# Optimization experiments

Hardware: AMD Instinct MI355X
Metric: run time of the kernel (lower is better)

The kernel has to match this reference:

```python
import math
import jax, jax.numpy as jnp
import numpy as np

EPS = 1e-5
D_MODEL, N_HEADS, D_HEAD = 512, 8, 64


def make_signed_quant(num_bits):
    Qn = -2 ** (num_bits - 1)
    Qp = 2 ** (num_bits - 1) - 1

    @jax.custom_vjp
    def quant(x, alpha):
        a = jnp.maximum(alpha, EPS)
        return jnp.clip(jnp.round(x / a), Qn, Qp) * a

    def fwd(x, alpha):
        a = jnp.maximum(alpha, EPS)
        return jnp.clip(jnp.round(x / a), Qn, Qp) * a, (x, a)

    def bwd(res, g):
        x, a = res
        qw = x / a
        small = (qw < Qn).astype(g.dtype)
        big = (qw > Qp).astype(g.dtype)
        mid = 1.0 - small - big
        gs = 1.0 / math.sqrt(x.size * Qp)
        ga = jnp.sum((small * Qn + big * Qp + mid * (jnp.round(qw) - qw)) * g) * gs
        return mid * g, ga.reshape(())

    quant.defvjp(fwd, bwd)
    return quant


def make_unsigned_quant(num_bits):
    Qp = 2 ** num_bits - 1

    @jax.custom_vjp
    def quant(x, alpha):
        a = jnp.maximum(alpha, EPS)
        mn = jnp.min(x)
        return jnp.clip(jnp.round((x - mn) / a), 0, Qp) * a + mn

    def fwd(x, alpha):
        a = jnp.maximum(alpha, EPS)
        mn = jnp.min(x)
        return jnp.clip(jnp.round((x - mn) / a), 0, Qp) * a + mn, (x - mn, a)

    def bwd(res, g):
        xs, a = res
        qw = xs / a
        small = (qw < 0).astype(g.dtype)
        big = (qw > Qp).astype(g.dtype)
        mid = 1.0 - small - big
        gs = 1.0 / math.sqrt(xs.size * Qp)
        ga = jnp.sum((big * Qp + mid * (jnp.round(qw) - qw)) * g) * gs
        return mid * g, ga.reshape(())

    quant.defvjp(fwd, bwd)
    return quant


def _bwn_body(w):
    # layerwise BWN: sign(w - mean(w)) * mean(|w|)
    m = jnp.mean(jnp.abs(w))
    e = jnp.mean(w)
    return jnp.sign(w - e) * m


@jax.custom_vjp
def bwn(w):
    return _bwn_body(w)


def _bwn_fwd(w):
    return _bwn_body(w), None


def _bwn_bwd(_, g):
    return (g,)  # straight-through


bwn.defvjp(_bwn_fwd, _bwn_bwd)

sig4 = make_signed_quant(4)
sig8 = make_signed_quant(8)  # the output QuantizeLinear uses default input_bits=8
uns4 = make_unsigned_quant(4)


def layernorm(x, g, b):
    mu = jnp.mean(x, axis=-1, keepdims=True)
    var = jnp.var(x, axis=-1, keepdims=True)
    return (x - mu) / jnp.sqrt(var + 1e-5) * g + b


def attention_forward(q, k, v, Wq, Wk, Wv, Wo, bq, bk, bv, ln_g, ln_b,
                      aq_in, ak_in, av_in, a_cq, a_ck, a_cv, a_cattn, ao_in):
    B, S, _ = q.shape
    # QuantizeLinear: 4-bit elastic act quant + BWN binary weights, NO bias; then LearnableBias add
    Q = sig4(q, aq_in) @ bwn(Wq).T + bq
    K = sig4(k, ak_in) @ bwn(Wk).T + bk
    V = sig4(v, av_in) @ bwn(Wv).T + bv

    def split(x):  # [B,S,H*d] -> [B,H,S,d]
        return jnp.transpose(x.reshape(B, -1, N_HEADS, D_HEAD), (0, 2, 1, 3))

    Q, K, V = split(Q), split(K), split(V)
    Q = sig4(Q, a_cq)
    K = sig4(K, a_ck)
    V = sig4(V, a_cv)
    scores = jnp.einsum('bhqd,bhkd->bhqk', Q, K) / math.sqrt(D_HEAD)
    # NOTE: original calls scores.masked_fill(mask==0, -1e9) WITHOUT assignment,
    # so the mask has no effect on the math; replicated faithfully.
    attn = jax.nn.softmax(scores, axis=-1)
    attn = uns4(attn, a_cattn)
    ctx = jnp.einsum('bhqk,bhkd->bhqd', attn, V)
    # faithful to original `.view(B, S, H*d)` on the [B,H,S,d] tensor (no head transpose)
    ctx = ctx.reshape(B, S, N_HEADS * D_HEAD)
    out = sig8(ctx, ao_in) @ bwn(Wo).T
    return layernorm(q + out, ln_g, ln_b), scores


def setup_inputs() -> dict:
    key = jax.random.key(0)
    ks = jax.random.split(key, 8)
    B, S, D = 4, 1024, 512
    f = jnp.float32
    return {
        'q': jax.random.normal(ks[0], (B, S, D), f),
        'k': jax.random.normal(ks[1], (B, S, D), f),
        'v': jax.random.normal(ks[2], (B, S, D), f),
        'mask': jnp.ones((B, 1, S, S), jnp.int32),
        'Wq': jax.random.normal(ks[3], (D, D), f) * 0.02,
        'Wk': jax.random.normal(ks[4], (D, D), f) * 0.02,
        'Wv': jax.random.normal(ks[5], (D, D), f) * 0.02,
        'Wo': jax.random.normal(ks[6], (D, D), f) * 0.02,
        'bq': jnp.zeros((D,), f),
        'bk': jnp.zeros((D,), f),
        'bv': jnp.zeros((D,), f),
        'ln_g': jnp.ones((D,), f),
        'ln_b': jnp.zeros((D,), f),
        'aq_in': jnp.asarray(0.5, f),
        'ak_in': jnp.asarray(0.5, f),
        'av_in': jnp.asarray(0.5, f),
        'a_cq': jnp.asarray(0.2, f),
        'a_ck': jnp.asarray(0.2, f),
        'a_cv': jnp.asarray(0.2, f),
        'a_cattn': jnp.asarray(0.002, f),
        'ao_in': jnp.asarray(0.01, f),
    }


def reference(q, k, v, mask, Wq, Wk, Wv, Wo, bq, bk, bv, ln_g, ln_b,
              aq_in, ak_in, av_in, a_cq, a_ck, a_cv, a_cattn, ao_in):
    # mask is structurally unused (original masked_fill is not in-place and discarded)
    return attention_forward(q, k, v, Wq, Wk, Wv, Wo, bq, bk, bv, ln_g, ln_b,
                             aq_in, ak_in, av_in, a_cq, a_ck, a_cv, a_cattn, ao_in)
```

## Files before the change

### kernel.cpp

```cpp
#include <hip/hip_runtime.h>
#include <math.h>
#include <stdint.h>

#define EPSQ 1e-5f
#define WELEM 262144
#define OUT0N 2097152

#define O_WSUM   0
#define O_WABS   16
#define O_MN     32
#define O_COLSUM 64
#define O_WSIGNS 16384
#define O_QLV    (O_WSIGNS + 8*WELEM)
#define O_CTXQ   O_QLV
#define O_KLV    (O_QLV + 4194304)
#define O_VLV    (O_KLV + 4194304)
#define O_KQ     (O_VLV + 4194304)
#define O_KK     (O_KQ + 4194304)
#define O_VT     (O_KK + 4194304)
#define O_RMAX   (O_VT + 4194304)
#define O_RSUM   (O_RMAX + 131072)
#define O_OUTB   (O_RSUM + 131072)
#define O_RCAND  O_OUTB

#define AS 72

typedef __bf16 bf16x8 __attribute__((ext_vector_type(8)));
typedef __bf16 bf16x4 __attribute__((ext_vector_type(4)));
typedef float  floatx4 __attribute__((ext_vector_type(4)));

struct pre2 { bf16x8 lo, hi; };
__device__ __forceinline__ pre2 ldb16(const __bf16* p) {
  pre2 r; r.lo = *(const bf16x8*)p; r.hi = *(const bf16x8*)(p + 8); return r;
}
__device__ __forceinline__ void stb16(__bf16* p, pre2 r) {
  *(bf16x8*)p = r.lo; *(bf16x8*)(p + 8) = r.hi;
}

__device__ __forceinline__ float clampf(float x, float lo, float hi) {
  return fminf(fmaxf(x, lo), hi);
}

__global__ void k_init(float* wsum, float* wabs, float* colsum) {
  int t = threadIdx.x;
  if (t < 4) { wsum[t] = 0.f; wabs[t] = 0.f; }
  for (int i = t; i < 2048; i += 256) colsum[i] = 0.f;
}

__global__ void k_wstats(const float* Wq, const float* Wk, const float* Wv, const float* Wo,
                         float* wsum, float* wabs) {
  __shared__ float s1[256], s2[256];
  int w = blockIdx.x >> 6;
  const float* W = (w == 0) ? Wq : (w == 1) ? Wk : (w == 2) ? Wv : Wo;
  int base = (blockIdx.x & 63) * 4096;
  float s = 0.f, sa = 0.f;
  for (int i = threadIdx.x; i < 4096; i += 256) {
    float x = W[base + i];
    s += x; sa += fabsf(x);
  }
  s1[threadIdx.x] = s; s2[threadIdx.x] = sa; __syncthreads();
  for (int o = 128; o > 0; o >>= 1) {
    if (threadIdx.x < o) { s1[threadIdx.x] += s1[threadIdx.x + o]; s2[threadIdx.x] += s2[threadIdx.x + o]; }
    __syncthreads();
  }
  if (threadIdx.x == 0) { atomicAdd(&wsum[w], s1[0]); atomicAdd(&wabs[w], s2[0]); }
}

__global__ void k_sign(const float* Wq, const float* Wk, const float* Wv, const float* Wo,
                       const float* wsum, __bf16* wsigns) {
  int idx = blockIdx.x * 256 + threadIdx.x;
  int w = idx >> 18;
  int pos = idx & (WELEM - 1);
  const float* W = (w == 0) ? Wq : (w == 1) ? Wk : (w == 2) ? Wv : Wo;
  float e = wsum[w] * (1.0f / 262144.0f);
  float x = W[pos];
  wsigns[idx] = (__bf16)(float)((x > e) - (x < e));
}

__global__ __launch_bounds__(256) void k_qx(
    const float* q, const float* kin, const float* vin,
    const float* aq, const float* ak, const float* av,
    __bf16* qlv, __bf16* klv, __bf16* vlv) {
  int z = blockIdx.y;
  const float* X = (z == 0) ? q : (z == 1) ? kin : vin;
  const float* ap = (z == 0) ? aq : (z == 1) ? ak : av;
  __bf16* O = (z == 0) ? qlv : (z == 1) ? klv : vlv;
  float a = fmaxf(ap[0], EPSQ);
  size_t i = ((size_t)blockIdx.x * 256 + threadIdx.x) * 8;
  float4 x0 = *(const float4*)&X[i];
  float4 x1 = *(const float4*)&X[i + 4];
  bf16x8 o = { (__bf16)clampf(rintf(x0.x / a), -8.f, 7.f),
               (__bf16)clampf(rintf(x0.y / a), -8.f, 7.f),
               (__bf16)clampf(rintf(x0.z / a), -8.f, 7.f),
               (__bf16)clampf(rintf(x0.w / a), -8.f, 7.f),
               (__bf16)clampf(rintf(x1.x / a), -8.f, 7.f),
               (__bf16)clampf(rintf(x1.y / a), -8.f, 7.f),
               (__bf16)clampf(rintf(x1.z / a), -8.f, 7.f),
               (__bf16)clampf(rintf(x1.w / a), -8.f, 7.f) };
  *(bf16x8*)&O[i] = o;
}

__global__ __launch_bounds__(256) void k_proj(
    const __bf16* qlv, const __bf16* klv, const __bf16* vlv,
    const float* bq, const float* bk, const float* bv,
    const float* aq, const float* ak, const float* av,
    const float* acq, const float* ack, const float* acv,
    const __bf16* wsigns, const float* wabs,
    __bf16* kqo, __bf16* kko, __bf16* vto, float* colsum) {
  __shared__ __align__(16) __bf16 As[64][AS];
  __shared__ __align__(16) __bf16 Bs[64][AS];
  int z = blockIdx.z;
  const __bf16* X   = (z == 0) ? qlv : (z == 1) ? klv : vlv;
  const float* bias = (z == 0) ? bq  : (z == 1) ? bk  : bv;
  const float* aip  = (z == 0) ? aq  : (z == 1) ? ak  : av;
  const float* ahp  = (z == 0) ? acq : (z == 1) ? ack : acv;
  float a_in = fmaxf(aip[0], EPSQ);
  float a_hd = fmaxf(ahp[0], EPSQ);
  float m_w  = wabs[z] * (1.0f / 262144.0f);
  const __bf16* S = wsigns + (size_t)z * WELEM;

  int n0 = blockIdx.x * 64;
  int f0 = blockIdx.y * 64;
  int t = threadIdx.x;
  int lane = t & 63, w = t >> 6, quad = lane >> 4, l16 = lane & 15;
  int e16 = (t & 3) * 16, mrow = t >> 2;
  const __bf16* ap = &X[(size_t)(n0 + mrow) * 512 + e16];
  const __bf16* bp = &S[(size_t)(f0 + mrow) * 512 + e16];
  floatx4 acc[4];
#pragma unroll
  for (int nt = 0; nt < 4; ++nt) acc[nt] = (floatx4){0.f, 0.f, 0.f, 0.f};

  pre2 pa = ldb16(ap), pb = ldb16(bp);
  for (int k0 = 0; k0 < 512; k0 += 64) {
    if (k0) __syncthreads();
    stb16(&As[mrow][e16], pa);
    stb16(&Bs[mrow][e16], pb);
    if (k0 + 64 < 512) { pa = ldb16(ap + k0 + 64); pb = ldb16(bp + k0 + 64); }
    __syncthreads();
#pragma unroll
    for (int kh = 0; kh < 64; kh += 32) {
      bf16x8 a = *(const bf16x8*)&As[w * 16 + l16][kh + quad * 8];
#pragma unroll
      for (int nt = 0; nt < 4; ++nt) {
        bf16x8 b = *(const bf16x8*)&Bs[nt * 16 + l16][kh + quad * 8];
        acc[nt] = __builtin_amdgcn_mfma_f32_16x16x32_bf16(a, b, acc[nt], 0, 0, 0);
      }
    }
  }
  float s_am = a_in * m_w;
  if (z != 2) {
    __bf16* outp = (z == 0) ? kqo : kko;
#pragma unroll
    for (int nt = 0; nt < 4; ++nt) {
      int f = f0 + nt * 16 + l16;
      int h = f >> 6, dd = f & 63;
      float bia = bias[f];
#pragma unroll
      for (int r = 0; r < 4; ++r) {
        int n = n0 + w * 16 + quad * 4 + r;
        int b = n >> 10, srow = n & 1023;
        float P = s_am * acc[nt][r] + bia;
        float hq = clampf(rintf(P / a_hd), -8.f, 7.f);
        outp[(size_t)((b * 8 + h) * 1024 + srow) * 64 + dd] = (__bf16)hq;
      }
    }
  } else {
    int b = n0 >> 10;
    int srow0 = (n0 & 1023) + w * 16 + quad * 4;
#pragma unroll
    for (int nt = 0; nt < 4; ++nt) {
      int f = f0 + nt * 16 + l16;
      int h = f >> 6, dd = f & 63;
      int bh = b * 8 + h;
      float bia = bias[f];
      float part = 0.f;
      bf16x4 pack;
#pragma unroll
      for (int r = 0; r < 4; ++r) {
        float P = s_am * acc[nt][r] + bia;
        float hq = clampf(rintf(P / a_hd), -8.f, 7.f);
        pack[r] = (__bf16)hq;
        part += hq;
      }
      *(bf16x4*)&vto[((size_t)bh * 64 + dd) * 1024 + srow0] = pack;
      atomicAdd(&colsum[bh * 64 + dd], part);
    }
  }
}

__global__ __launch_bounds__(256) void k_qks(
    const __bf16* kq, const __bf16* kkv,
    const float* acq, const float* ack,
    float* scores, float* rmax, float* rsum, float* rcand) {
  __shared__ __align__(16) __bf16 As[64][AS];
  __shared__ __align__(16) __bf16 Bs[64][AS];
  int bh = blockIdx.y;
  int q0 = blockIdx.x * 64;
  const __bf16* A  = kq  + (size_t)bh * 65536;
  const __bf16* Bp = kkv + (size_t)bh * 65536;
  float* Sp = scores + ((size_t)bh * 1024 + q0) * 1024;
  int t = threadIdx.x;
  int lane = t & 63, w = t >> 6, quad = lane >> 4, l16 = lane & 15;
  int e16 = (t & 3) * 16, mrow = t >> 2;
  float sc = fmaxf(acq[0], EPSQ) * fmaxf(ack[0], EPSQ) * 0.125f;

  stb16(&As[mrow][e16], ldb16(&A[(q0 + mrow) * 64 + e16]));
  float m_run[4], l_run[4], mn_run[4];
#pragma unroll
  for (int rr = 0; rr < 4; ++rr) { m_run[rr] = -INFINITY; l_run[rr] = 0.f; mn_run[rr] = INFINITY; }

  pre2 pb = ldb16(&Bp[mrow * 64 + e16]);
  for (int ct = 0; ct < 16; ++ct) {
    if (ct) __syncthreads();
    stb16(&Bs[mrow][e16], pb);
    if (ct < 15) pb = ldb16(&Bp[((ct + 1) * 64 + mrow) * 64 + e16]);
    __syncthreads();
    floatx4 acc[4];
#pragma unroll
    for (int nt = 0; nt < 4; ++nt) acc[nt] = (floatx4){0.f, 0.f, 0.f, 0.f};
#pragma unroll
    for (int kh = 0; kh < 64; kh += 32) {
      bf16x8 a = *(const bf16x8*)&As[w * 16 + l16][kh + quad * 8];
#pragma unroll
      for (int nt = 0; nt < 4; ++nt) {
        bf16x8 b = *(const bf16x8*)&Bs[nt * 16 + l16][kh + quad * 8];
        acc[nt] = __builtin_amdgcn_mfma_f32_16x16x32_bf16(a, b, acc[nt], 0, 0, 0);
      }
    }
#pragma unroll
    for (int rr = 0; rr < 4; ++rr) {
      int row = w * 16 + quad * 4 + rr;
      float v[4];
#pragma unroll
      for (int nt = 0; nt < 4; ++nt) {
        v[nt] = sc * acc[nt][rr];
        Sp[(size_t)row * 1024 + ct * 64 + nt * 16 + l16] = v[nt];
      }
      float tmax = fmaxf(fmaxf(v[0], v[1]), fmaxf(v[2], v[3]));
      float tmin = fminf(fminf(v[0], v[1]), fminf(v[2], v[3]));
      mn_run[rr] = fminf(mn_run[rr], tmin);
      float mnew = fmaxf(m_run[rr], tmax);
      float s = 0.f;
#pragma unroll
      for (int nt = 0; nt < 4; ++nt) s += expf(v[nt] - mnew);
      l_run[rr] = l_run[rr] * expf(m_run[rr] - mnew) + s;
      m_run[rr] = mnew;
    }
  }
#pragma unroll
  for (int o = 1; o < 16; o <<= 1) {
#pragma unroll
    for (int rr = 0; rr < 4; ++rr) {
      float mo = __shfl_xor(m_run[rr], o);
      float lo = __shfl_xor(l_run[rr], o);
      float mnew = fmaxf(m_run[rr], mo);
      l_run[rr] = l_run[rr] * expf(m_run[rr] - mnew) + lo * expf(mo - mnew);
      m_run[rr] = mnew;
      mn_run[rr] = fminf(mn_run[rr], __shfl_xor(mn_run[rr], o));
    }
  }
  if (l16 == 0) {
#pragma unroll
    for (int rr = 0; rr < 4; ++rr) {
      int r = bh * 1024 + q0 + w * 16 + quad * 4 + rr;
      rmax[r] = m_run[rr];
      rsum[r] = l_run[rr];
      rcand[r] = expf(mn_run[rr] - m_run[rr]) * (1.0f / l_run[rr]);
    }
  }
}

__global__ __launch_bounds__(1024) void k_minred(const float* rcand, float* mnf) {
  __shared__ float red[1024];
  float mn = INFINITY;
  for (int i = threadIdx.x; i < 32768; i += 1024) mn = fminf(mn, rcand[i]);
  red[threadIdx.x] = mn; __syncthreads();
  for (int o = 512; o > 0; o >>= 1) {
    if (threadIdx.x < o) red[threadIdx.x] = fminf(red[threadIdx.x], red[threadIdx.x + o]);
    __syncthreads();
  }
  if (threadIdx.x == 0) mnf[0] = red[0];
}

__global__ __launch_bounds__(256) void k_pv(
    const float* scores, const float* rmax, const float* rsum,
    const float* mnf, const float* colsum, const __bf16* vt,
    const float* acattn, const float* acv, const float* ao,
    __bf16* ctxq) {
  __shared__ __align__(16) __bf16 As[32][AS];
  __shared__ __align__(16) __bf16 Bs[64][AS];
  int bh = blockIdx.y;
  int m0 = blockIdx.x * 32;
  float mn = mnf[0];
  float a_att = fmaxf(acattn[0], EPSQ);
  float a_v   = fmaxf(acv[0], EPSQ);
  float a_o   = fmaxf(ao[0], EPSQ);
  const float* Sp  = scores + (size_t)bh * 1048576;
  const __bf16* Vt = vt + (size_t)bh * 65536;
  int t = threadIdx.x;
  int lane = t & 63, w = t >> 6, quad = lane >> 4, l16 = lane & 15;
  int mt = w & 1, np = w >> 1;
  int c4 = (t & 15) * 4, mb = t >> 4;
  int e16 = (t & 3) * 16, mrow = t >> 2;
  float rm[2], rs[2];
#pragma unroll
  for (int j = 0; j < 2; ++j) {
    int r = bh * 1024 + m0 + mb + j * 16;
    rm[j] = rmax[r]; rs[j] = rsum[r];
  }
  floatx4 acc[2];
  acc[0] = (floatx4){0.f, 0.f, 0.f, 0.f};
  acc[1] = (floatx4){0.f, 0.f, 0.f, 0.f};

  float4 ps[2];
#pragma unroll
  for (int j = 0; j < 2; ++j)
    ps[j] = *(const float4*)&Sp[(size_t)(m0 + mb + j * 16) * 1024 + c4];
  pre2 pvb = ldb16(&Vt[(size_t)mrow * 1024 + e16]);

  for (int k0 = 0; k0 < 1024; k0 += 64) {
    if (k0) __syncthreads();
#pragma unroll
    for (int j = 0; j < 2; ++j) {
      float inv = 1.0f / rs[j];
      bf16x4 av = {
        (__bf16)clampf(rintf((expf(ps[j].x - rm[j]) * inv - mn) / a_att), 0.f, 15.f),
        (__bf16)clampf(rintf((expf(ps[j].y - rm[j]) * inv - mn) / a_att), 0.f, 15.f),
        (__bf16)clampf(rintf((expf(ps[j].z - rm[j]) * inv - mn) / a_att), 0.f, 15.f),
        (__bf16)clampf(rintf((expf(ps[j].w - rm[j]) * inv - mn) / a_att), 0.f, 15.f) };
      *(bf16x4*)&As[mb + j * 16][c4] = av;
    }
    stb16(&Bs[mrow][e16], pvb);
    if (k0 + 64 < 1024) {
#pragma unroll
      for (int j = 0; j < 2; ++j)
        ps[j] = *(const float4*)&Sp[(size_t)(m0 + mb + j * 16) * 1024 + k0 + 64 + c4];
      pvb = ldb16(&Vt[(size_t)mrow * 1024 + k0 + 64 + e16]);
    }
    __syncthreads();
#pragma unroll
    for (int kh = 0; kh < 64; kh += 32) {
      bf16x8 a = *(const bf16x8*)&As[mt * 16 + l16][kh + quad * 8];
#pragma unroll
      for (int j = 0; j < 2; ++j) {
        bf16x8 b = *(const bf16x8*)&Bs[(np * 2 + j) * 16 + l16][kh + quad * 8];
        acc[j] = __builtin_amdgcn_mfma_f32_16x16x32_bf16(a, b, acc[j], 0, 0, 0);
      }
    }
  }
  float sc  = a_att * a_v;
  float mnv = mn * a_v;
  int b = bh >> 3, h = bh & 7;
#pragma unroll
  for (int j = 0; j < 2; ++j) {
    int dd = (np * 2 + j) * 16 + l16;
    float cs = colsum[bh * 64 + dd];
#pragma unroll
    for (int r = 0; r < 4; ++r) {
      int srow = m0 + mt * 16 + quad * 4 + r;
      float ctx = sc * acc[j][r] + mnv * cs;
      float c8 = clampf(rintf(ctx / a_o), -128.f, 127.f);
      ctxq[(size_t)b * 524288 + (size_t)(h * 128 + (srow >> 3)) * 512 + (srow & 7) * 64 + dd] = (__bf16)c8;
    }
  }
}

__global__ __launch_bounds__(256) void k_outg(
    const __bf16* ctxq, const __bf16* signs_o,
    const float* wabs, const float* ao, float* outb) {
  __shared__ __align__(16) __bf16 As[64][AS];
  __shared__ __align__(16) __bf16 Bs[64][AS];
  int n0 = blockIdx.x * 64, f0 = blockIdx.y * 64;
  int t = threadIdx.x;
  int lane = t & 63, w = t >> 6, quad = lane >> 4, l16 = lane & 15;
  int e16 = (t & 3) * 16, mrow = t >> 2;
  const __bf16* ap = &ctxq[(size_t)(n0 + mrow) * 512 + e16];
  const __bf16* bp = &signs_o[(size_t)(f0 + mrow) * 512 + e16];
  floatx4 acc[4];
#pragma unroll
  for (int nt = 0; nt < 4; ++nt) acc[nt] = (floatx4){0.f, 0.f, 0.f, 0.f};
  pre2 pa = ldb16(ap), pb = ldb16(bp);
  for (int k0 = 0; k0 < 512; k0 += 64) {
    if (k0) __syncthreads();
    stb16(&As[mrow][e16], pa);
    stb16(&Bs[mrow][e16], pb);
    if (k0 + 64 < 512) { pa = ldb16(ap + k0 + 64); pb = ldb16(bp + k0 + 64); }
    __syncthreads();
#pragma unroll
    for (int kh = 0; kh < 64; kh += 32) {
      bf16x8 a = *(const bf16x8*)&As[w * 16 + l16][kh + quad * 8];
#pragma unroll
      for (int nt = 0; nt < 4; ++nt) {
        bf16x8 b = *(const bf16x8*)&Bs[nt * 16 + l16][kh + quad * 8];
        acc[nt] = __builtin_amdgcn_mfma_f32_16x16x32_bf16(a, b, acc[nt], 0, 0, 0);
      }
    }
  }
  float scale = fmaxf(ao[0], EPSQ) * (wabs[3] * (1.0f / 262144.0f));
#pragma unroll
  for (int nt = 0; nt < 4; ++nt)
#pragma unroll
    for (int r = 0; r < 4; ++r)
      outb[(size_t)(n0 + w * 16 + quad * 4 + r) * 512 + f0 + nt * 16 + l16] = scale * acc[nt][r];
}

__global__ __launch_bounds__(256) void k_ln(
    const float* q, const float* outb, const float* g, const float* bb, float* out0) {
  __shared__ float red[256];
  int r = blockIdx.x, t = threadIdx.x;
  const float* qp = q + (size_t)r * 512;
  const float* op = outb + (size_t)r * 512;
  float y0 = qp[t] + op[t];
  float y1 = qp[t + 256] + op[t + 256];
  red[t] = y0 + y1; __syncthreads();
  for (int o = 128; o > 0; o >>= 1) { if (t < o) red[t] += red[t + o]; __syncthreads(); }
  float mu = red[0] * (1.0f / 512.0f); __syncthreads();
  float d0 = y0 - mu, d1 = y1 - mu;
  red[t] = d0 * d0 + d1 * d1; __syncthreads();
  for (int o = 128; o > 0; o >>= 1) { if (t < o) red[t] += red[t + o]; __syncthreads(); }
  float var = red[0] * (1.0f / 512.0f);
  float den = sqrtf(var + 1e-5f);
  out0[(size_t)r * 512 + t]       = d0 / den * g[t] + bb[t];
  out0[(size_t)r * 512 + t + 256] = d1 / den * g[t + 256] + bb[t + 256];
}

extern "C" void kernel_launch(void* const* d_in, const int* in_sizes, int n_in,
                              void* d_out, int out_size, void* d_ws, size_t ws_size,
                              hipStream_t stream) {
  const float* q   = (const float*)d_in[0];
  const float* k   = (const float*)d_in[1];
  const float* v   = (const float*)d_in[2];
  const float* Wq  = (const float*)d_in[4];
  const float* Wk  = (const float*)d_in[5];
  const float* Wv  = (const float*)d_in[6];
  const float* Wo  = (const float*)d_in[7];
  const float* bq  = (const float*)d_in[8];
  const float* bk  = (const float*)d_in[9];
  const float* bv  = (const float*)d_in[10];
  const float* lng = (const float*)d_in[11];
  const float* lnb = (const float*)d_in[12];
  const float* aq  = (const float*)d_in[13];
  const float* ak  = (const float*)d_in[14];
  const float* av  = (const float*)d_in[15];
  const float* acq = (const float*)d_in[16];
  const float* ack = (const float*)d_in[17];
  const float* acv = (const float*)d_in[18];
  const float* aca = (const float*)d_in[19];
  const float* ao  = (const float*)d_in[20];

  char* ws = (char*)d_ws;
  float*  wsum   = (float*)(ws + O_WSUM);
  float*  wabs   = (float*)(ws + O_WABS);
  float*  mnf    = (float*)(ws + O_MN);
  float*  colsum = (float*)(ws + O_COLSUM);
  __bf16* wsigns = (__bf16*)(ws + O_WSIGNS);
  __bf16* qlv    = (__bf16*)(ws + O_QLV);
  __bf16* klv    = (__bf16*)(ws + O_KLV);
  __bf16* vlv    = (__bf16*)(ws + O_VLV);
  __bf16* kqb    = (__bf16*)(ws + O_KQ);
  __bf16* kkb    = (__bf16*)(ws + O_KK);
  __bf16* vtb    = (__bf16*)(ws + O_VT);
  float*  rmax   = (float*)(ws + O_RMAX);
  float*  rsum   = (float*)(ws + O_RSUM);
  float*  rcand  = (float*)(ws + O_RCAND);
  __bf16* ctxq   = (__bf16*)(ws + O_CTXQ);
  float*  outb   = (float*)(ws + O_OUTB);

  float* out0   = (float*)d_out;
  float* scores = (float*)d_out + OUT0N;

  k_init<<<1, 256, 0, stream>>>(wsum, wabs, colsum);
  k_wstats<<<256, 256, 0, stream>>>(Wq, Wk, Wv, Wo, wsum, wabs);
  k_sign<<<4096, 256, 0, stream>>>(Wq, Wk, Wv, Wo, wsum, wsigns);
  k_qx<<<dim3(1024, 3), 256, 0, stream>>>(q, k, v, aq, ak, av, qlv, klv, vlv);
  k_proj<<<dim3(64, 8, 3), 256, 0, stream>>>(qlv, klv, vlv, bq, bk, bv, aq, ak, av,
                                             acq, ack, acv, wsigns, wabs,
                                             kqb, kkb, vtb, colsum);
  k_qks<<<dim3(16, 32), 256, 0, stream>>>(kqb, kkb, acq, ack, scores, rmax, rsum, rcand);
  k_minred<<<1, 1024, 0, stream>>>(rcand, mnf);
  k_pv<<<dim3(32, 32), 256, 0, stream>>>(scores, rmax, rsum, mnf, colsum, vtb,
                                         aca, acv, ao, ctxq);
  k_outg<<<dim3(64, 8), 256, 0, stream>>>(ctxq, wsigns + 3 * WELEM, wabs, ao, outb);
  k_ln<<<4096, 256, 0, stream>>>(q, outb, lng, lnb, out0);
}
```

Before: 349.3 us.

## Recompute QK scores in PV kernel and fuse global min via atomicMin

```diff
diff --git a/kernel.cpp b/kernel.cpp
--- a/kernel.cpp
+++ b/kernel.cpp
@@ -21,7 +21,6 @@
 #define O_RMAX   (O_VT + 4194304)
 #define O_RSUM   (O_RMAX + 131072)
 #define O_OUTB   (O_RSUM + 131072)
-#define O_RCAND  O_OUTB
 
 #define AS 72
 
@@ -41,9 +40,10 @@
   return fminf(fmaxf(x, lo), hi);
 }
 
-__global__ void k_init(float* wsum, float* wabs, float* colsum) {
+__global__ void k_init(float* wsum, float* wabs, float* colsum, unsigned int* mnbits) {
   int t = threadIdx.x;
   if (t < 4) { wsum[t] = 0.f; wabs[t] = 0.f; }
+  if (t == 0) mnbits[0] = 0x7f800000u;
   for (int i = t; i < 2048; i += 256) colsum[i] = 0.f;
 }
 
@@ -191,9 +191,10 @@
 __global__ __launch_bounds__(256) void k_qks(
     const __bf16* kq, const __bf16* kkv,
     const float* acq, const float* ack,
-    float* scores, float* rmax, float* rsum, float* rcand) {
+    float* scores, float* rmax, float* rsum, unsigned int* mnbits) {
   __shared__ __align__(16) __bf16 As[64][AS];
   __shared__ __align__(16) __bf16 Bs[64][AS];
+  __shared__ float redmin[16];
   int bh = blockIdx.y;
   int q0 = blockIdx.x * 64;
   const __bf16* A  = kq  + (size_t)bh * 65536;
@@ -260,95 +261,112 @@
     }
   }
   if (l16 == 0) {
+    float cand = INFINITY;
 #pragma unroll
     for (int rr = 0; rr < 4; ++rr) {
       int r = bh * 1024 + q0 + w * 16 + quad * 4 + rr;
       rmax[r] = m_run[rr];
       rsum[r] = l_run[rr];
-      rcand[r] = expf(mn_run[rr] - m_run[rr]) * (1.0f / l_run[rr]);
-    }
-  }
-}
-
-__global__ __launch_bounds__(1024) void k_minred(const float* rcand, float* mnf) {
-  __shared__ float red[1024];
-  float mn = INFINITY;
-  for (int i = threadIdx.x; i < 32768; i += 1024) mn = fminf(mn, rcand[i]);
-  red[threadIdx.x] = mn; __syncthreads();
-  for (int o = 512; o > 0; o >>= 1) {
-    if (threadIdx.x < o) red[threadIdx.x] = fminf(red[threadIdx.x], red[threadIdx.x + o]);
-    __syncthreads();
-  }
-  if (threadIdx.x == 0) mnf[0] = red[0];
+      cand = fminf(cand, expf(mn_run[rr] - m_run[rr]) * (1.0f / l_run[rr]));
+    }
+    redmin[w * 4 + quad] = cand;
+  }
+  __syncthreads();
+  if (t == 0) {
+    float c = redmin[0];
+#pragma unroll
+    for (int i = 1; i < 16; ++i) c = fminf(c, redmin[i]);
+    atomicMin(mnbits, __float_as_uint(c));
+  }
 }
 
 __global__ __launch_bounds__(256) void k_pv(
-    const float* scores, const float* rmax, const float* rsum,
+    const __bf16* kq, const __bf16* kkv,
+    const float* rmax, const float* rsum,
     const float* mnf, const float* colsum, const __bf16* vt,
+    const float* acq, const float* ack,
     const float* acattn, const float* acv, const float* ao,
     __bf16* ctxq) {
+  __shared__ __align__(16) __bf16 Ks[64][AS];
+  __shared__ __align__(16) __bf16 Vs[64][AS];
   __shared__ __align__(16) __bf16 As[32][AS];
-  __shared__ __align__(16) __bf16 Bs[64][AS];
   int bh = blockIdx.y;
   int m0 = blockIdx.x * 32;
-  float mn = mnf[0];
+  float mn    = mnf[0];
   float a_att = fmaxf(acattn[0], EPSQ);
   float a_v   = fmaxf(acv[0], EPSQ);
   float a_o   = fmaxf(ao[0], EPSQ);
-  const float* Sp  = scores + (size_t)bh * 1048576;
-  const __bf16* Vt = vt + (size_t)bh * 65536;
+  float sc    = fmaxf(acq[0], EPSQ) * fmaxf(ack[0], EPSQ) * 0.125f;
+  const __bf16* Qp = kq  + (size_t)bh * 65536;
+  const __bf16* Kp = kkv + (size_t)bh * 65536;
+  const __bf16* Vt = vt  + (size_t)bh * 65536;
   int t = threadIdx.x;
   int lane = t & 63, w = t >> 6, quad = lane >> 4, l16 = lane & 15;
+  int e16 = (t & 3) * 16, mrow = t >> 2;
   int mt = w & 1, np = w >> 1;
-  int c4 = (t & 15) * 4, mb = t >> 4;
-  int e16 = (t & 3) * 16, mrow = t >> 2;
-  float rm[2], rs[2];
-#pragma unroll
-  for (int j = 0; j < 2; ++j) {
-    int r = bh * 1024 + m0 + mb + j * 16;
-    rm[j] = rmax[r]; rs[j] = rsum[r];
-  }
+
+  bf16x8 qa[2][2];
+#pragma unroll
+  for (int mh = 0; mh < 2; ++mh)
+#pragma unroll
+    for (int kh2 = 0; kh2 < 2; ++kh2)
+      qa[mh][kh2] = *(const bf16x8*)&Qp[(size_t)(m0 + mh * 16 + l16) * 64 + kh2 * 32 + quad * 8];
+
+  float rm[2][4], inv[2][4];
+#pragma unroll
+  for (int mh = 0; mh < 2; ++mh)
+#pragma unroll
+    for (int r = 0; r < 4; ++r) {
+      int rr = bh * 1024 + m0 + mh * 16 + quad * 4 + r;
+      rm[mh][r]  = rmax[rr];
+      inv[mh][r] = 1.0f / rsum[rr];
+    }
+
   floatx4 acc[2];
   acc[0] = (floatx4){0.f, 0.f, 0.f, 0.f};
   acc[1] = (floatx4){0.f, 0.f, 0.f, 0.f};
 
-  float4 ps[2];
-#pragma unroll
-  for (int j = 0; j < 2; ++j)
-    ps[j] = *(const float4*)&Sp[(size_t)(m0 + mb + j * 16) * 1024 + c4];
-  pre2 pvb = ldb16(&Vt[(size_t)mrow * 1024 + e16]);
-
-  for (int k0 = 0; k0 < 1024; k0 += 64) {
-    if (k0) __syncthreads();
-#pragma unroll
-    for (int j = 0; j < 2; ++j) {
-      float inv = 1.0f / rs[j];
-      bf16x4 av = {
-        (__bf16)clampf(rintf((expf(ps[j].x - rm[j]) * inv - mn) / a_att), 0.f, 15.f),
-        (__bf16)clampf(rintf((expf(ps[j].y - rm[j]) * inv - mn) / a_att), 0.f, 15.f),
-        (__bf16)clampf(rintf((expf(ps[j].z - rm[j]) * inv - mn) / a_att), 0.f, 15.f),
-        (__bf16)clampf(rintf((expf(ps[j].w - rm[j]) * inv - mn) / a_att), 0.f, 15.f) };
-      *(bf16x4*)&As[mb + j * 16][c4] = av;
-    }
-    stb16(&Bs[mrow][e16], pvb);
-    if (k0 + 64 < 1024) {
-#pragma unroll
-      for (int j = 0; j < 2; ++j)
-        ps[j] = *(const float4*)&Sp[(size_t)(m0 + mb + j * 16) * 1024 + k0 + 64 + c4];
-      pvb = ldb16(&Vt[(size_t)mrow * 1024 + k0 + 64 + e16]);
-    }
+  pre2 kpre = ldb16(&Kp[(size_t)mrow * 64 + e16]);
+  pre2 vpre = ldb16(&Vt[(size_t)mrow * 1024 + e16]);
+  for (int ct = 0; ct < 16; ++ct) {
+    if (ct) __syncthreads();
+    stb16(&Ks[mrow][e16], kpre);
+    stb16(&Vs[mrow][e16], vpre);
+    if (ct < 15) {
+      kpre = ldb16(&Kp[(size_t)((ct + 1) * 64 + mrow) * 64 + e16]);
+      vpre = ldb16(&Vt[(size_t)mrow * 1024 + (ct + 1) * 64 + e16]);
+    }
+    __syncthreads();
+    floatx4 s2[2];
+    s2[0] = (floatx4){0.f, 0.f, 0.f, 0.f};
+    s2[1] = (floatx4){0.f, 0.f, 0.f, 0.f};
+#pragma unroll
+    for (int kh2 = 0; kh2 < 2; ++kh2) {
+      bf16x8 b = *(const bf16x8*)&Ks[w * 16 + l16][kh2 * 32 + quad * 8];
+#pragma unroll
+      for (int mh = 0; mh < 2; ++mh)
+        s2[mh] = __builtin_amdgcn_mfma_f32_16x16x32_bf16(qa[mh][kh2], b, s2[mh], 0, 0, 0);
+    }
+#pragma unroll
+    for (int mh = 0; mh < 2; ++mh)
+#pragma unroll
+      for (int r = 0; r < 4; ++r) {
+        float p = expf(sc * s2[mh][r] - rm[mh][r]) * inv[mh][r];
+        As[mh * 16 + quad * 4 + r][w * 16 + l16] =
+            (__bf16)clampf(rintf((p - mn) / a_att), 0.f, 15.f);
+      }
     __syncthreads();
 #pragma unroll
     for (int kh = 0; kh < 64; kh += 32) {
       bf16x8 a = *(const bf16x8*)&As[mt * 16 + l16][kh + quad * 8];
 #pragma unroll
       for (int j = 0; j < 2; ++j) {
-        bf16x8 b = *(const bf16x8*)&Bs[(np * 2 + j) * 16 + l16][kh + quad * 8];
+        bf16x8 b = *(const bf16x8*)&Vs[(np * 2 + j) * 16 + l16][kh + quad * 8];
         acc[j] = __builtin_amdgcn_mfma_f32_16x16x32_bf16(a, b, acc[j], 0, 0, 0);
       }
     }
   }
-  float sc  = a_att * a_v;
+  float scf = a_att * a_v;
   float mnv = mn * a_v;
   int b = bh >> 3, h = bh & 7;
 #pragma unroll
@@ -358,7 +376,7 @@
 #pragma unroll
     for (int r = 0; r < 4; ++r) {
       int srow = m0 + mt * 16 + quad * 4 + r;
-      float ctx = sc * acc[j][r] + mnv * cs;
+      float ctx = scf * acc[j][r] + mnv * cs;
       float c8 = clampf(rintf(ctx / a_o), -128.f, 127.f);
       ctxq[(size_t)b * 524288 + (size_t)(h * 128 + (srow >> 3)) * 512 + (srow & 7) * 64 + dd] = (__bf16)c8;
     }
@@ -462,24 +480,23 @@
   __bf16* vtb    = (__bf16*)(ws + O_VT);
   float*  rmax   = (float*)(ws + O_RMAX);
   float*  rsum   = (float*)(ws + O_RSUM);
-  float*  rcand  = (float*)(ws + O_RCAND);
   __bf16* ctxq   = (__bf16*)(ws + O_CTXQ);
   float*  outb   = (float*)(ws + O_OUTB);
 
   float* out0   = (float*)d_out;
   float* scores = (float*)d_out + OUT0N;
 
-  k_init<<<1, 256, 0, stream>>>(wsum, wabs, colsum);
+  k_init<<<1, 256, 0, stream>>>(wsum, wabs, colsum, (unsigned int*)mnf);
   k_wstats<<<256, 256, 0, stream>>>(Wq, Wk, Wv, Wo, wsum, wabs);
   k_sign<<<4096, 256, 0, stream>>>(Wq, Wk, Wv, Wo, wsum, wsigns);
   k_qx<<<dim3(1024, 3), 256, 0, stream>>>(q, k, v, aq, ak, av, qlv, klv, vlv);
   k_proj<<<dim3(64, 8, 3), 256, 0, stream>>>(qlv, klv, vlv, bq, bk, bv, aq, ak, av,
                                              acq, ack, acv, wsigns, wabs,
                                              kqb, kkb, vtb, colsum);
-  k_qks<<<dim3(16, 32), 256, 0, stream>>>(kqb, kkb, acq, ack, scores, rmax, rsum, rcand);
-  k_minred<<<1, 1024, 0, stream>>>(rcand, mnf);
-  k_pv<<<dim3(32, 32), 256, 0, stream>>>(scores, rmax, rsum, mnf, colsum, vtb,
-                                         aca, acv, ao, ctxq);
+  k_qks<<<dim3(16, 32), 256, 0, stream>>>(kqb, kkb, acq, ack, scores, rmax, rsum,
+                                          (unsigned int*)mnf);
+  k_pv<<<dim3(32, 32), 256, 0, stream>>>(kqb, kkb, rmax, rsum, mnf, colsum, vtb,
+                                         acq, ack, aca, acv, ao, ctxq);
   k_outg<<<dim3(64, 8), 256, 0, stream>>>(ctxq, wsigns + 3 * WELEM, wabs, ao, outb);
   k_ln<<<4096, 256, 0, stream>>>(q, outb, lng, lnb, out0);
 }
```

After: 348.1 us. No clear change (-0.3%).
